# Performance work log

Measured on AMD Instinct MI355X. Metric: run time of the kernel, lower is better.

Reference implementation:

```python
import jax, jax.numpy as jnp
import numpy as np
from jax.scipy.special import logsumexp

B, T, D, H, K = 64, 800, 80, 128, 39  # batch, frames, feat dim, LSTM hidden/dir, num phones


def setup_inputs() -> dict:
    key = jax.random.key(0)
    ks = jax.random.split(key, 16)
    s = 0.1
    inp = {
        "features": jax.random.normal(ks[0], (B, T, D), jnp.float32),
        "lengths": jax.random.randint(ks[1], (B,), T // 2, T + 1, dtype=jnp.int32),
        "labels": jax.random.randint(ks[2], (B, T), 0, K, dtype=jnp.int32),
        # BiLSTM params (PyTorch layout: W_ih (4H,D), W_hh (4H,H); gate order i,f,g,o)
        "Wih_f": jax.random.normal(ks[3], (4 * H, D), jnp.float32) * s,
        "Whh_f": jax.random.normal(ks[4], (4 * H, H), jnp.float32) * s,
        "bih_f": jax.random.normal(ks[5], (4 * H,), jnp.float32) * s,
        "bhh_f": jax.random.normal(ks[6], (4 * H,), jnp.float32) * s,
        "Wih_b": jax.random.normal(ks[7], (4 * H, D), jnp.float32) * s,
        "Whh_b": jax.random.normal(ks[8], (4 * H, H), jnp.float32) * s,
        "bih_b": jax.random.normal(ks[9], (4 * H,), jnp.float32) * s,
        "bhh_b": jax.random.normal(ks[10], (4 * H,), jnp.float32) * s,
        # emission projection Linear(2H -> K)
        "Wp": jax.random.normal(ks[11], (K, 2 * H), jnp.float32) * s,
        "bp": jax.random.normal(ks[12], (K,), jnp.float32) * s,
        # CRF params (pytorch-crf init: U(-0.1, 0.1))
        "start_t": jax.random.uniform(ks[13], (K,), jnp.float32, -0.1, 0.1),
        "end_t": jax.random.uniform(ks[14], (K,), jnp.float32, -0.1, 0.1),
        "trans": jax.random.uniform(ks[15], (K, K), jnp.float32, -0.1, 0.1),
    }
    return inp


def _lstm(x, Wih, Whh, bih, bhh, reverse):
    """Single-direction LSTM over padded batch. x: (B,T,D) -> (B,T,H)."""
    nB, nT, _ = x.shape
    nH = Whh.shape[1]
    xW = jnp.swapaxes(x @ Wih.T + (bih + bhh), 0, 1)  # (T,B,4H)

    def step(carry, g):
        h, c = carry
        g = g + h @ Whh.T
        i, f, gg, o = jnp.split(g, 4, axis=-1)
        c = jax.nn.sigmoid(f) * c + jax.nn.sigmoid(i) * jnp.tanh(gg)
        h = jax.nn.sigmoid(o) * jnp.tanh(c)
        return (h, c), h

    init = (jnp.zeros((nB, nH), x.dtype), jnp.zeros((nB, nH), x.dtype))
    _, hs = jax.lax.scan(step, init, xW, reverse=reverse)
    return jnp.swapaxes(hs, 0, 1)  # (B,T,H)


def _crf_nll(emissions, labels, lengths, start_t, end_t, trans):
    """pytorch-crf: -mean log-likelihood. emissions (B,T,K), labels (B,T)."""
    nB, nT, nK = emissions.shape
    mask = (jnp.arange(nT)[None, :] < lengths[:, None])  # (B,T)
    mf = mask.astype(emissions.dtype)
    bidx = jnp.arange(nB)

    # --- numerator: score of gold path ---
    num = start_t[labels[:, 0]] + emissions[bidx, 0, labels[:, 0]]
    tr = trans[labels[:, :-1], labels[:, 1:]]  # (B,T-1)
    em = jnp.take_along_axis(emissions[:, 1:], labels[:, 1:, None], axis=2)[..., 0]
    num = num + ((tr + em) * mf[:, 1:]).sum(axis=1)
    last_tags = jnp.take_along_axis(labels, (lengths - 1)[:, None], axis=1)[:, 0]
    num = num + end_t[last_tags]

    # --- denominator: forward algorithm ---
    alpha0 = start_t[None, :] + emissions[:, 0]  # (B,K)
    em_rest = jnp.swapaxes(emissions[:, 1:], 0, 1)  # (T-1,B,K)
    m_rest = jnp.swapaxes(mask[:, 1:], 0, 1)  # (T-1,B)

    def step(alpha, inputs):
        em_t, m_t = inputs
        nxt = logsumexp(alpha[:, :, None] + trans[None] + em_t[:, None, :], axis=1)
        return jnp.where(m_t[:, None], nxt, alpha), None

    alpha, _ = jax.lax.scan(step, alpha0, (em_rest, m_rest))
    denom = logsumexp(alpha + end_t[None, :], axis=1)

    return -(num - denom).mean()


def reference(features, lengths, labels, Wih_f, Whh_f, bih_f, bhh_f,
              Wih_b, Whh_b, bih_b, bhh_b, Wp, bp, start_t, end_t, trans):
    h_f = _lstm(features, Wih_f, Whh_f, bih_f, bhh_f, reverse=False)
    h_b = _lstm(features, Wih_b, Whh_b, bih_b, bhh_b, reverse=True)
    hidden = jnp.concatenate([h_f, h_b], axis=-1)  # (B,T,2H)
    emissions = hidden @ Wp.T + bp  # (B,T,K)
    return _crf_nll(emissions, labels, lengths, start_t, end_t, trans)
```

## Files before the change

### kernel.cpp

```cpp
#include <hip/hip_runtime.h>
#include <cstddef>
#include <cstdint>

#define B_ 64
#define T_ 800
#define D_ 80
#define H_ 128
#define K_ 39
#define BT_ (B_ * T_)

#define NL2E_  (-1.44269504f)
#define N2L2E_ (-2.88539008f)

typedef _Float16 h2_t  __attribute__((ext_vector_type(2)));
typedef _Float16 f16x8 __attribute__((ext_vector_type(8)));
typedef float    f32x4 __attribute__((ext_vector_type(4)));
typedef uint32_t u32x4 __attribute__((ext_vector_type(4)));

__device__ __forceinline__ float fdot2_(h2_t a, h2_t b, float c) {
#if __has_builtin(__builtin_amdgcn_fdot2)
  return __builtin_amdgcn_fdot2(a, b, c, false);
#else
  return c + (float)a.x * (float)b.x + (float)a.y * (float)b.y;
#endif
}

__device__ __forceinline__ h2_t asH2u_(uint32_t u) { return __builtin_bit_cast(h2_t, u); }

__device__ __forceinline__ float ex2_(float x) {
#if __has_builtin(__builtin_amdgcn_exp2f)
  return __builtin_amdgcn_exp2f(x);
#else
  return __builtin_exp2f(x);
#endif
}
__device__ __forceinline__ float rcpf_(float x) {
#if __has_builtin(__builtin_amdgcn_rcpf)
  return __builtin_amdgcn_rcpf(x);
#else
  return 1.0f / x;
#endif
}
__device__ __forceinline__ float tanhf_(float x) { return 2.0f / (1.0f + __expf(-2.0f * x)) - 1.0f; }

__device__ __forceinline__ float laneb_(float v, int lane) {
  return __builtin_bit_cast(float, __builtin_amdgcn_readlane(__builtin_bit_cast(int, v), lane));
}
__device__ __forceinline__ uint32_t lanebu_(uint32_t v, int lane) {
  return (uint32_t)__builtin_amdgcn_readlane((int)v, lane);
}

__device__ __forceinline__ float dppswap1_(float v) {
  return __builtin_bit_cast(float,
    __builtin_amdgcn_mov_dpp(__builtin_bit_cast(int, v), 0xB1, 0xF, 0xF, true));
}

__device__ __forceinline__ void barrier_lds_() {
  asm volatile("s_waitcnt lgkmcnt(0)" ::: "memory");
  __builtin_amdgcn_s_barrier();
}

__device__ __forceinline__ void rows_of_(int tid, int& unit, int& role, int& r0, int& r1) {
  const int w = tid >> 6, L = tid & 63;
  unit = w * 32 + (L >> 1);
  role = L & 1;
  r0 = role * H_ + unit;
  r1 = 2 * H_ + role * H_ + unit;
}

__global__ __launch_bounds__(256, 1)
void xw_kernel(const float* __restrict__ x,
               const float* __restrict__ Wih_f, const float* __restrict__ Wih_b,
               _Float16* __restrict__ xw)
{
  const int dir = blockIdx.x & 1;
  const int mc  = blockIdx.x >> 1;
  const float* W = dir ? Wih_b : Wih_f;

  const int tid  = threadIdx.x;
  const int w    = tid >> 6;
  const int lane = tid & 63;
  const int lm   = lane & 15;
  const int quad = lane >> 4;
  const int selw = w >> 1;
  const int rolw = w & 1;

  f16x8 Bf[8][3];
  #pragma unroll
  for (int nt = 0; nt < 8; ++nt) {
    const int r = w * 128 + nt * 16 + lm;
    const float fac = (r >= 256 && r < 384) ? N2L2E_ : NL2E_;
    #pragma unroll
    for (int kt = 0; kt < 3; ++kt) {
      const int kb = kt * 32 + quad * 8;
      #pragma unroll
      for (int j = 0; j < 8; ++j) {
        const int k = kb + j;
        Bf[nt][kt][j] = (k < D_) ? (_Float16)(fac * W[(size_t)r * D_ + k]) : (_Float16)0.0f;
      }
    }
  }

  __shared__ alignas(16) _Float16 xs[128 * 96];
  for (int i = tid; i < 128 * 96; i += 256) xs[i] = (_Float16)0.0f;

  for (int cc = 0; cc < 4; ++cc) {
    const int base = mc * 512 + cc * 128;
    __syncthreads();
    {
      const float4* src = (const float4*)(x + (size_t)base * D_);
      for (int i = tid; i < 128 * D_ / 4; i += 256) {
        float4 v = src[i];
        const int row = i / 20, col = (i % 20) * 4;
        h2_t p0, p1;
        p0.x = (_Float16)v.x; p0.y = (_Float16)v.y;
        p1.x = (_Float16)v.z; p1.y = (_Float16)v.w;
        uint2 pk;
        pk.x = __builtin_bit_cast(uint32_t, p0);
        pk.y = __builtin_bit_cast(uint32_t, p1);
        *(uint2*)&xs[row * 96 + col] = pk;
      }
    }
    __syncthreads();

    #pragma unroll
    for (int mt = 0; mt < 8; ++mt) {
      f16x8 Af[3];
      #pragma unroll
      for (int kt = 0; kt < 3; ++kt)
        Af[kt] = *(const f16x8*)&xs[(mt * 16 + lm) * 96 + kt * 32 + quad * 8];

      f32x4 acc[8];
      #pragma unroll
      for (int nt = 0; nt < 8; ++nt) acc[nt] = (f32x4){0.f, 0.f, 0.f, 0.f};
      #pragma unroll
      for (int kt = 0; kt < 3; ++kt)
        #pragma unroll
        for (int nt = 0; nt < 8; ++nt)
          acc[nt] = __builtin_amdgcn_mfma_f32_16x16x32_f16(Af[kt], Bf[nt][kt], acc[nt], 0, 0, 0);

      #pragma unroll
      for (int nt = 0; nt < 8; ++nt) {
        const int unit = nt * 16 + lm;
        const int ptid = (unit >> 5) * 64 + (unit & 31) * 2 + rolw;
        #pragma unroll
        for (int rg = 0; rg < 4; ++rg) {
          const int bt = base + mt * 16 + quad * 4 + rg;
          xw[((size_t)dir * BT_ + bt) * 512 + ptid * 2 + selw] = (_Float16)acc[nt][rg];
        }
      }
    }
  }
}

template<int USE_XW>
__global__ __launch_bounds__(256, 1)
void lstm_kernel(const float* __restrict__ x,
                 const float* __restrict__ Wih_f, const float* __restrict__ Whh_f,
                 const float* __restrict__ bih_f, const float* __restrict__ bhh_f,
                 const float* __restrict__ Wih_b, const float* __restrict__ Whh_b,
                 const float* __restrict__ bih_b, const float* __restrict__ bhh_b,
                 const _Float16* __restrict__ xw,
                 _Float16* __restrict__ hcat)
{
  const int bb  = blockIdx.x & 63;
  const int dir = blockIdx.x >> 6;
  const float* Whh = dir ? Whh_b : Whh_f;
  const float* Wih = dir ? Wih_b : Wih_f;
  const float* bih = dir ? bih_b : bih_f;
  const float* bhh = dir ? bhh_b : bhh_f;

  const int tid  = threadIdx.x;
  const int lane = tid & 63;
  int unit, role, r0, r1; rows_of_(tid, unit, role, r0, r1);
  const float s0 = NL2E_;
  const float s1 = role ? NL2E_ : N2L2E_;
  const float qk2 = role ? 0.0f : -1.0f;

  h2_t w0[64], w1[64];
  #pragma unroll
  for (int j = 0; j < 64; ++j) {
    float2 a = *(const float2*)(Whh + (size_t)r0 * H_ + 2 * j);
    float2 d = *(const float2*)(Whh + (size_t)r1 * H_ + 2 * j);
    w0[j].x = (_Float16)(s0 * a.x); w0[j].y = (_Float16)(s0 * a.y);
    w1[j].x = (_Float16)(s1 * d.x); w1[j].y = (_Float16)(s1 * d.y);
  }
  h2_t wx0[40], wx1[40];
  if (!USE_XW) {
    #pragma unroll
    for (int i = 0; i < 40; ++i) {
      float2 a = *(const float2*)(Wih + (size_t)r0 * D_ + 2 * i);
      float2 d = *(const float2*)(Wih + (size_t)r1 * D_ + 2 * i);
      wx0[i].x = (_Float16)(s0 * a.x); wx0[i].y = (_Float16)(s0 * a.y);
      wx1[i].x = (_Float16)(s1 * d.x); wx1[i].y = (_Float16)(s1 * d.y);
    }
  }
  const float bias0 = s0 * (bih[r0] + bhh[r0]);
  const float bias1 = s1 * (bih[r1] + bhh[r1]);

  __shared__ alignas(16) _Float16 hsf[2][H_];
  __shared__ uint32_t xs2[2][64];

  if (tid < H_) hsf[0][tid] = (_Float16)0.0f;
  if (!USE_XW && tid < 64) { xs2[0][tid] = 0u; xs2[1][tid] = 0u; }
  float c = 0.0f;

  const uint32_t* xwdu = (const uint32_t*)xw + ((size_t)dir * BT_ + (size_t)bb * T_) * 256;
  const float*    xb   = x + (size_t)bb * T_ * D_;
  _Float16*       hb   = hcat + (size_t)bb * T_ * (2 * H_) + dir * H_;

  _Float16* hbp = hb + (size_t)(dir ? (T_ - 1) : 0) * (2 * H_);
  const ptrdiff_t hstep = dir ? -(2 * H_) : (2 * H_);
  int xoff = (dir ? (T_ - 3) : 2) * 256 + tid;
  const int xstep = dir ? -256 : 256;

  uint32_t xwA = 0u, xwB = 0u;
  h2_t xpend; xpend.x = (_Float16)0.f; xpend.y = (_Float16)0.f;
  {
    const int tq0 = dir ? (T_ - 1) : 0;
    const int tq1 = dir ? (T_ - 2) : 1;
    if (USE_XW) {
      xwA = xwdu[(size_t)tq0 * 256 + tid];
      xwB = xwdu[(size_t)tq1 * 256 + tid];
    } else if (tid < 40) {
      float2 v0 = *(const float2*)(xb + (size_t)tq0 * D_ + 2 * tid);
      h2_t p; p.x = (_Float16)v0.x; p.y = (_Float16)v0.y;
      xs2[0][tid] = __builtin_bit_cast(uint32_t, p);
      float2 v1 = *(const float2*)(xb + (size_t)tq1 * D_ + 2 * tid);
      xpend.x = (_Float16)v1.x; xpend.y = (_Float16)v1.y;
    }
  }
  __syncthreads();

  auto step = [&](int tt, int par, uint32_t& xwreg) {
    float a0, a1, a2, a3, b0, b1, b2, b3;
    if (USE_XW) {
      const h2_t xv = asH2u_(xwreg);
      a0 = bias0 + (float)xv.x;
      b0 = bias1 + (float)xv.y;
      a1 = a2 = a3 = 0.f; b1 = b2 = b3 = 0.f;
      xwreg = xwdu[xoff];
    } else {
      a0 = bias0; b0 = bias1;
      a1 = a2 = a3 = 0.f; b1 = b2 = b3 = 0.f;
      if (tid < 40) {
        xs2[par ^ 1][tid] = __builtin_bit_cast(uint32_t, xpend);
        const int ttc = (tt + 2 < T_) ? (tt + 2) : (T_ - 1);
        const int tq2 = dir ? (T_ - 1 - ttc) : ttc;
        float2 v = *(const float2*)(xb + (size_t)tq2 * D_ + 2 * tid);
        xpend.x = (_Float16)v.x; xpend.y = (_Float16)v.y;
      }
      uint32_t xreg = xs2[par][lane];
      #pragma unroll
      for (int j = 0; j < 40; j += 4) {
        h2_t q0 = asH2u_(lanebu_(xreg, j));
        h2_t q1 = asH2u_(lanebu_(xreg, j + 1));
        h2_t q2 = asH2u_(lanebu_(xreg, j + 2));
        h2_t q3 = asH2u_(lanebu_(xreg, j + 3));
        a0 = fdot2_(wx0[j],     q0, a0); b0 = fdot2_(wx1[j],     q0, b0);
        a1 = fdot2_(wx0[j + 1], q1, a1); b1 = fdot2_(wx1[j + 1], q1, b1);
        a2 = fdot2_(wx0[j + 2], q2, a2); b2 = fdot2_(wx1[j + 2], q2, b2);
        a3 = fdot2_(wx0[j + 3], q3, a3); b3 = fdot2_(wx1[j + 3], q3, b3);
      }
    }

    const u32x4* hq = (const u32x4*)hsf[par];
    #pragma unroll
    for (int g = 0; g < 16; ++g) {
      const u32x4 hv = hq[g];
      a0 = fdot2_(w0[4 * g + 0], asH2u_(hv[0]), a0);
      b0 = fdot2_(w1[4 * g + 0], asH2u_(hv[0]), b0);
      a1 = fdot2_(w0[4 * g + 1], asH2u_(hv[1]), a1);
      b1 = fdot2_(w1[4 * g + 1], asH2u_(hv[1]), b1);
      a2 = fdot2_(w0[4 * g + 2], asH2u_(hv[2]), a2);
      b2 = fdot2_(w1[4 * g + 2], asH2u_(hv[2]), b2);
      a3 = fdot2_(w0[4 * g + 3], asH2u_(hv[3]), a3);
      b3 = fdot2_(w1[4 * g + 3], asH2u_(hv[3]), b3);
    }
    const float ga = (a0 + a1) + (a2 + a3);
    const float gb = (b0 + b1) + (b2 + b3);

    const float ea = ex2_(ga);
    const float sg = rcpf_(1.0f + ea);
    const float gbc = fminf(fmaxf(gb, -34.6f), 34.6f);
    const float eb = ex2_(gbc);
    const float qv = fmaf(qk2, eb, 1.0f) * rcpf_(1.0f + eb);
    const float ex = dppswap1_(sg * qv);
    c = fmaf(sg, c, ex);
    const float hn = qv * tanhf_(c);
    if (role) {
      hsf[par ^ 1][unit] = (_Float16)hn;
      hbp[unit] = (_Float16)hn;
    }
    hbp += hstep;
    if (tt + 3 < T_) xoff += xstep;
    barrier_lds_();
  };

  for (int tb = 0; tb < T_; tb += 2) {
    step(tb,     0, xwA);
    step(tb + 1, 1, xwB);
  }
}

__global__ __launch_bounds__(256, 1)
void emis_kernel(const _Float16* __restrict__ hcat,
                 const float* __restrict__ Wp, const float* __restrict__ bp,
                 float* __restrict__ em)
{
  const int tid  = threadIdx.x;
  const int w    = tid >> 6;
  const int lane = tid & 63;
  const int lm   = lane & 15;
  const int quad = lane >> 4;

  f16x8 Bf[3][8];
  float bias[3];
  #pragma unroll
  for (int nt = 0; nt < 3; ++nt) {
    const int n = nt * 16 + lm;
    const bool valid = n < K_;
    bias[nt] = valid ? bp[n] : 0.0f;
    #pragma unroll
    for (int kt = 0; kt < 8; ++kt) {
      const int kb = kt * 32 + quad * 8;
      #pragma unroll
      for (int j = 0; j < 8; ++j)
        Bf[nt][kt][j] = valid ? (_Float16)Wp[(size_t)n * 256 + kb + j] : (_Float16)0.0f;
    }
  }

  #pragma unroll
  for (int q = 0; q < 4; ++q) {
    const int mt  = blockIdx.x * 16 + w * 4 + q;
    const int bt0 = mt * 16;

    f16x8 Af[8];
    const _Float16* ab = hcat + ((size_t)bt0 + lm) * 256;
    #pragma unroll
    for (int kt = 0; kt < 8; ++kt)
      Af[kt] = *(const f16x8*)(ab + kt * 32 + quad * 8);

    f32x4 acc[3];
    #pragma unroll
    for (int nt = 0; nt < 3; ++nt) acc[nt] = (f32x4){0.f, 0.f, 0.f, 0.f};
    #pragma unroll
    for (int kt = 0; kt < 8; ++kt)
      #pragma unroll
      for (int nt = 0; nt < 3; ++nt)
        acc[nt] = __builtin_amdgcn_mfma_f32_16x16x32_f16(Af[kt], Bf[nt][kt], acc[nt], 0, 0, 0);

    #pragma unroll
    for (int nt = 0; nt < 3; ++nt) {
      const int n = nt * 16 + lm;
      if (n < K_) {
        #pragma unroll
        for (int rg = 0; rg < 4; ++rg) {
          const int row = bt0 + quad * 4 + rg;
          em[(size_t)row * K_ + n] = acc[nt][rg] + bias[nt];
        }
      }
    }
  }
}

__global__ __launch_bounds__(256)
void crf_dn_kernel(const float* __restrict__ em,
                   const int* __restrict__ labels, const int* __restrict__ lengths,
                   const float* __restrict__ start_t, const float* __restrict__ end_t,
                   const float* __restrict__ trans,
                   float* __restrict__ dn)
{
  const int b    = blockIdx.x;
  const int tid  = threadIdx.x;
  const int wv   = tid >> 6;
  const int lane = tid & 63;
  const int len  = lengths[b];
  const float* emb = em + (size_t)b * T_ * K_;

  __shared__ float s_num[3];
  __shared__ float s_den;
  __shared__ alignas(16) float vbuf[64];

  if (wv == 0) {
    float et[K_];
    #pragma unroll
    for (int j = 0; j < K_; ++j)
      et[j] = (lane < K_) ? __expf(trans[j * K_ + lane]) : 0.0f;

    float a0 = (lane < K_) ? (start_t[lane] + emb[lane]) : -1e30f;
    float m = a0;
    #pragma unroll
    for (int off = 32; off > 0; off >>= 1) m = fmaxf(m, __shfl_xor(m, off));
    float v = __expf(a0 - m);
    float off_acc = m;
    vbuf[lane] = 0.0f;

    auto ldc = [&](int t) -> float {
      const int tc = (t < len) ? t : (len - 1);
      return (lane < K_) ? emb[(size_t)tc * K_ + lane] : 0.0f;
    };

    float eA = ldc(1), eB = ldc(2), eC = ldc(3), eD = ldc(4);
    float eE = ldc(5), eF = ldc(6), eG = ldc(7), eH = ldc(8);

    auto stepden = [&](float& ereg, int tt) {
      const float emc = ereg;
      ereg = ldc(tt + 8);
      if (tt < len) {
        vbuf[lane] = v;
        asm volatile("s_waitcnt lgkmcnt(0)" ::: "memory");
        const float4* vq = (const float4*)vbuf;
        float s0 = 0.f, s1 = 0.f, s2 = 0.f, s3 = 0.f;
        #pragma unroll
        for (int g = 0; g < 9; ++g) {
          const float4 q = vq[g];
          s0 = fmaf(q.x, et[4 * g],     s0);
          s1 = fmaf(q.y, et[4 * g + 1], s1);
          s2 = fmaf(q.z, et[4 * g + 2], s2);
          s3 = fmaf(q.w, et[4 * g + 3], s3);
        }
        const float4 q9 = vq[9];
        s0 = fmaf(q9.x, et[36], s0);
        s1 = fmaf(q9.y, et[37], s1);
        s2 = fmaf(q9.z, et[38], s2);
        v = ((s0 + s1) + (s2 + s3)) * __expf(emc);
        if ((tt & 1) == 0) {
          const float sc = laneb_(v, 0);
          v *= 1.0f / sc;
          off_acc += __logf(sc);
        }
      }
    };

    for (int t = 1; t < len; t += 8) {
      stepden(eA, t);     stepden(eB, t + 1);
      stepden(eC, t + 2); stepden(eD, t + 3);
      stepden(eE, t + 4); stepden(eF, t + 5);
      stepden(eG, t + 6); stepden(eH, t + 7);
    }

    float w = (lane < K_) ? v * __expf(end_t[lane]) : 0.0f;
    #pragma unroll
    for (int off = 32; off > 0; off >>= 1) w += __shfl_xor(w, off);
    if (lane == 0) s_den = off_acc + __logf(w);
  } else {
    const int idx = tid - 64;
    float acc = 0.0f;
    for (int t = 1 + idx; t < len; t += 192) {
      const int lp = labels[b * T_ + t - 1];
      const int lc = labels[b * T_ + t];
      acc += trans[lp * K_ + lc] + emb[(size_t)t * K_ + lc];
    }
    if (tid == 64) {
      const int l0 = labels[b * T_];
      const int ll = labels[b * T_ + len - 1];
      acc += start_t[l0] + emb[l0] + end_t[ll];
    }
    #pragma unroll
    for (int off = 32; off > 0; off >>= 1) acc += __shfl_xor(acc, off);
    if (lane == 0) s_num[wv - 1] = acc;
  }
  __syncthreads();
  if (tid == 0) dn[b] = s_den - (s_num[0] + s_num[1] + s_num[2]);
}

__global__ void finalize_kernel(const float* __restrict__ dn, float* __restrict__ out)
{
  const int tid = threadIdx.x;
  float v = dn[tid];
  #pragma unroll
  for (int off = 32; off > 0; off >>= 1) v += __shfl_down(v, off);
  if (tid == 0) out[0] = v * (1.0f / 64.0f);
}

extern "C" void kernel_launch(void* const* d_in, const int* in_sizes, int n_in,
                              void* d_out, int out_size, void* d_ws, size_t ws_size,
                              hipStream_t stream)
{
  (void)in_sizes; (void)n_in; (void)out_size;
  const float* features = (const float*)d_in[0];
  const int*   lengths  = (const int*)d_in[1];
  const int*   labels   = (const int*)d_in[2];
  const float* Wih_f = (const float*)d_in[3];
  const float* Whh_f = (const float*)d_in[4];
  const float* bih_f = (const float*)d_in[5];
  const float* bhh_f = (const float*)d_in[6];
  const float* Wih_b = (const float*)d_in[7];
  const float* Whh_b = (const float*)d_in[8];
  const float* bih_b = (const float*)d_in[9];
  const float* bhh_b = (const float*)d_in[10];
  const float* Wp      = (const float*)d_in[11];
  const float* bp      = (const float*)d_in[12];
  const float* start_t = (const float*)d_in[13];
  const float* end_t   = (const float*)d_in[14];
  const float* trans   = (const float*)d_in[15];
  float* out = (float*)d_out;

  char* wsc = (char*)d_ws;
  _Float16* hcatH = (_Float16*)wsc;
  float*    em    = (float*)(wsc + 26214400);
  float*    dn    = (float*)(wsc + 26214400 + 7987200);
  _Float16* xwH   = (_Float16*)(wsc + 34202112);
  const bool big  = ws_size >= (size_t)34202112 + 104857600;

  if (big) {
    hipLaunchKernelGGL(xw_kernel, dim3(200), dim3(256), 0, stream,
                       features, Wih_f, Wih_b, xwH);
    hipLaunchKernelGGL((lstm_kernel<1>), dim3(2 * B_), dim3(256), 0, stream,
                       features, Wih_f, Whh_f, bih_f, bhh_f,
                       Wih_b, Whh_b, bih_b, bhh_b, xwH, hcatH);
  } else {
    hipLaunchKernelGGL((lstm_kernel<0>), dim3(2 * B_), dim3(256), 0, stream,
                       features, Wih_f, Whh_f, bih_f, bhh_f,
                       Wih_b, Whh_b, bih_b, bhh_b, xwH, hcatH);
  }
  hipLaunchKernelGGL(emis_kernel, dim3(BT_ / 256), dim3(256), 0, stream,
                     hcatH, Wp, bp, em);
  hipLaunchKernelGGL(crf_dn_kernel, dim3(B_), dim3(256), 0, stream,
                     em, labels, lengths, start_t, end_t, trans, dn);
  hipLaunchKernelGGL(finalize_kernel, dim3(1), dim3(64), 0, stream,
                     dn, out);
}
```

Before: 788.8 us.

## Share hidden-state LDS reads across lane quads via DPP and broadcast CRF alpha via readlane

In the LSTM recurrence, each lane of a 4-lane quad now reads only one quarter of the hidden vector from LDS. The other quarters arrive through DPP quad permutes, and the Whh fragments are reordered per lane to match. This cuts LDS read traffic per step on the serial critical path, at the cost of 48 extra DPP moves per step and a permuted weight layout. In the CRF forward pass, the LDS store, wait and vector reload of alpha is replaced by readlane broadcasts, which removes an LDS round trip per time step but adds scalar readlanes.

```diff
diff --git a/kernel.cpp b/kernel.cpp
--- a/kernel.cpp
+++ b/kernel.cpp
@@ -53,6 +53,11 @@
 __device__ __forceinline__ float dppswap1_(float v) {
   return __builtin_bit_cast(float,
     __builtin_amdgcn_mov_dpp(__builtin_bit_cast(int, v), 0xB1, 0xF, 0xF, true));
+}
+
+template<int CTRL>
+__device__ __forceinline__ uint32_t dppu_(uint32_t v) {
+  return (uint32_t)__builtin_amdgcn_mov_dpp((int)v, CTRL, 0xF, 0xF, true);
 }
 
 __device__ __forceinline__ void barrier_lds_() {
@@ -172,18 +177,24 @@
 
   const int tid  = threadIdx.x;
   const int lane = tid & 63;
+  const int Q    = lane & 3;
   int unit, role, r0, r1; rows_of_(tid, unit, role, r0, r1);
   const float s0 = NL2E_;
   const float s1 = role ? NL2E_ : N2L2E_;
   const float qk2 = role ? 0.0f : -1.0f;
 
-  h2_t w0[64], w1[64];
+  h2_t wp0[64], wp1[64];
   #pragma unroll
-  for (int j = 0; j < 64; ++j) {
-    float2 a = *(const float2*)(Whh + (size_t)r0 * H_ + 2 * j);
-    float2 d = *(const float2*)(Whh + (size_t)r1 * H_ + 2 * j);
-    w0[j].x = (_Float16)(s0 * a.x); w0[j].y = (_Float16)(s0 * a.y);
-    w1[j].x = (_Float16)(s1 * d.x); w1[j].y = (_Float16)(s1 * d.y);
+  for (int r = 0; r < 4; ++r) {
+    const int ch = Q ^ r;
+    #pragma unroll
+    for (int jj = 0; jj < 16; ++jj) {
+      const int j = ch * 16 + jj;
+      float2 a = *(const float2*)(Whh + (size_t)r0 * H_ + 2 * j);
+      float2 d = *(const float2*)(Whh + (size_t)r1 * H_ + 2 * j);
+      wp0[r * 16 + jj].x = (_Float16)(s0 * a.x); wp0[r * 16 + jj].y = (_Float16)(s0 * a.y);
+      wp1[r * 16 + jj].x = (_Float16)(s1 * d.x); wp1[r * 16 + jj].y = (_Float16)(s1 * d.y);
+    }
   }
   h2_t wx0[40], wx1[40];
   if (!USE_XW) {
@@ -233,16 +244,16 @@
   __syncthreads();
 
   auto step = [&](int tt, int par, uint32_t& xwreg) {
-    float a0, a1, a2, a3, b0, b1, b2, b3;
+    float a[4], b[4];
     if (USE_XW) {
       const h2_t xv = asH2u_(xwreg);
-      a0 = bias0 + (float)xv.x;
-      b0 = bias1 + (float)xv.y;
-      a1 = a2 = a3 = 0.f; b1 = b2 = b3 = 0.f;
+      a[0] = bias0 + (float)xv.x;
+      b[0] = bias1 + (float)xv.y;
+      a[1] = a[2] = a[3] = 0.f; b[1] = b[2] = b[3] = 0.f;
       xwreg = xwdu[xoff];
     } else {
-      a0 = bias0; b0 = bias1;
-      a1 = a2 = a3 = 0.f; b1 = b2 = b3 = 0.f;
+      a[0] = bias0; b[0] = bias1;
+      a[1] = a[2] = a[3] = 0.f; b[1] = b[2] = b[3] = 0.f;
       if (tid < 40) {
         xs2[par ^ 1][tid] = __builtin_bit_cast(uint32_t, xpend);
         const int ttc = (tt + 2 < T_) ? (tt + 2) : (T_ - 1);
@@ -257,28 +268,47 @@
         h2_t q1 = asH2u_(lanebu_(xreg, j + 1));
         h2_t q2 = asH2u_(lanebu_(xreg, j + 2));
         h2_t q3 = asH2u_(lanebu_(xreg, j + 3));
-        a0 = fdot2_(wx0[j],     q0, a0); b0 = fdot2_(wx1[j],     q0, b0);
-        a1 = fdot2_(wx0[j + 1], q1, a1); b1 = fdot2_(wx1[j + 1], q1, b1);
-        a2 = fdot2_(wx0[j + 2], q2, a2); b2 = fdot2_(wx1[j + 2], q2, b2);
-        a3 = fdot2_(wx0[j + 3], q3, a3); b3 = fdot2_(wx1[j + 3], q3, b3);
+        a[0] = fdot2_(wx0[j],     q0, a[0]); b[0] = fdot2_(wx1[j],     q0, b[0]);
+        a[1] = fdot2_(wx0[j + 1], q1, a[1]); b[1] = fdot2_(wx1[j + 1], q1, b[1]);
+        a[2] = fdot2_(wx0[j + 2], q2, a[2]); b[2] = fdot2_(wx1[j + 2], q2, b[2]);
+        a[3] = fdot2_(wx0[j + 3], q3, a[3]); b[3] = fdot2_(wx1[j + 3], q3, b[3]);
       }
     }
 
     const u32x4* hq = (const u32x4*)hsf[par];
-    #pragma unroll
-    for (int g = 0; g < 16; ++g) {
-      const u32x4 hv = hq[g];
-      a0 = fdot2_(w0[4 * g + 0], asH2u_(hv[0]), a0);
-      b0 = fdot2_(w1[4 * g + 0], asH2u_(hv[0]), b0);
-      a1 = fdot2_(w0[4 * g + 1], asH2u_(hv[1]), a1);
-      b1 = fdot2_(w1[4 * g + 1], asH2u_(hv[1]), b1);
-      a2 = fdot2_(w0[4 * g + 2], asH2u_(hv[2]), a2);
-      b2 = fdot2_(w1[4 * g + 2], asH2u_(hv[2]), b2);
-      a3 = fdot2_(w0[4 * g + 3], asH2u_(hv[3]), a3);
-      b3 = fdot2_(w1[4 * g + 3], asH2u_(hv[3]), b3);
-    }
-    const float ga = (a0 + a1) + (a2 + a3);
-    const float gb = (b0 + b1) + (b2 + b3);
+    u32x4 ovr[4];
+    #pragma unroll
+    for (int reg = 0; reg < 4; ++reg) ovr[reg] = hq[Q * 4 + reg];
+
+    u32x4 x1[4], x2[4], x3[4];
+    #pragma unroll
+    for (int reg = 0; reg < 4; ++reg) {
+      #pragma unroll
+      for (int e = 0; e < 4; ++e) {
+        x1[reg][e] = dppu_<0xB1>(ovr[reg][e]);
+        x2[reg][e] = dppu_<0x4E>(ovr[reg][e]);
+        x3[reg][e] = dppu_<0x1B>(ovr[reg][e]);
+      }
+    }
+
+    #define HROUND_(HV, RB)                                        \
+      _Pragma("unroll")                                            \
+      for (int reg = 0; reg < 4; ++reg) {                          \
+        _Pragma("unroll")                                          \
+        for (int e = 0; e < 4; ++e) {                              \
+          const h2_t hh = asH2u_((HV)[reg][e]);                    \
+          a[e] = fdot2_(wp0[(RB) + reg * 4 + e], hh, a[e]);        \
+          b[e] = fdot2_(wp1[(RB) + reg * 4 + e], hh, b[e]);        \
+        }                                                          \
+      }
+    HROUND_(ovr, 0)
+    HROUND_(x1, 16)
+    HROUND_(x2, 32)
+    HROUND_(x3, 48)
+    #undef HROUND_
+
+    const float ga = (a[0] + a[1]) + (a[2] + a[3]);
+    const float gb = (b[0] + b[1]) + (b[2] + b[3]);
 
     const float ea = ex2_(ga);
     const float sg = rcpf_(1.0f + ea);
@@ -380,7 +410,6 @@
 
   __shared__ float s_num[3];
   __shared__ float s_den;
-  __shared__ alignas(16) float vbuf[64];
 
   if (wv == 0) {
     float et[K_];
@@ -394,7 +423,6 @@
     for (int off = 32; off > 0; off >>= 1) m = fmaxf(m, __shfl_xor(m, off));
     float v = __expf(a0 - m);
     float off_acc = m;
-    vbuf[lane] = 0.0f;
 
     auto ldc = [&](int t) -> float {
       const int tc = (t < len) ? t : (len - 1);
@@ -408,22 +436,18 @@
       const float emc = ereg;
       ereg = ldc(tt + 8);
       if (tt < len) {
-        vbuf[lane] = v;
-        asm volatile("s_waitcnt lgkmcnt(0)" ::: "memory");
-        const float4* vq = (const float4*)vbuf;
+        const float pv = v;
         float s0 = 0.f, s1 = 0.f, s2 = 0.f, s3 = 0.f;
         #pragma unroll
-        for (int g = 0; g < 9; ++g) {
-          const float4 q = vq[g];
-          s0 = fmaf(q.x, et[4 * g],     s0);
-          s1 = fmaf(q.y, et[4 * g + 1], s1);
-          s2 = fmaf(q.z, et[4 * g + 2], s2);
-          s3 = fmaf(q.w, et[4 * g + 3], s3);
+        for (int j = 0; j < 36; j += 4) {
+          s0 = fmaf(laneb_(pv, j),     et[j],     s0);
+          s1 = fmaf(laneb_(pv, j + 1), et[j + 1], s1);
+          s2 = fmaf(laneb_(pv, j + 2), et[j + 2], s2);
+          s3 = fmaf(laneb_(pv, j + 3), et[j + 3], s3);
         }
-        const float4 q9 = vq[9];
-        s0 = fmaf(q9.x, et[36], s0);
-        s1 = fmaf(q9.y, et[37], s1);
-        s2 = fmaf(q9.z, et[38], s2);
+        s0 = fmaf(laneb_(pv, 36), et[36], s0);
+        s1 = fmaf(laneb_(pv, 37), et[37], s1);
+        s2 = fmaf(laneb_(pv, 38), et[38], s2);
         v = ((s0 + s1) + (s2 + s3)) * __expf(emc);
         if ((tt & 1) == 0) {
           const float sc = laneb_(v, 0);
```

Result: faster. 749.0 us (-5.1%).

## Fuse input projection into LSTM kernel and use lane broadcasts in CRF recursion

Applied to the files above, without the earlier changes.

Removes the separate xw_kernel and has each LSTM block compute its own batch row's input projection with MFMA before the recurrence, writing into its own xw slice. This drops a kernel launch and lets the projection run inside the 128-block LSTM grid instead of a separate 200-block pass. The CRF forward step now gathers alpha with lane broadcasts instead of an LDS round trip, and renormalizes every fourth step instead of every second. The fused prologue serializes projection work per block on only 128 CUs. Less frequent renormalization carries some overflow risk.

```diff
diff --git a/kernel.cpp b/kernel.cpp
--- a/kernel.cpp
+++ b/kernel.cpp
@@ -66,91 +66,6 @@
   role = L & 1;
   r0 = role * H_ + unit;
   r1 = 2 * H_ + role * H_ + unit;
-}
-
-__global__ __launch_bounds__(256, 1)
-void xw_kernel(const float* __restrict__ x,
-               const float* __restrict__ Wih_f, const float* __restrict__ Wih_b,
-               _Float16* __restrict__ xw)
-{
-  const int dir = blockIdx.x & 1;
-  const int mc  = blockIdx.x >> 1;
-  const float* W = dir ? Wih_b : Wih_f;
-
-  const int tid  = threadIdx.x;
-  const int w    = tid >> 6;
-  const int lane = tid & 63;
-  const int lm   = lane & 15;
-  const int quad = lane >> 4;
-  const int selw = w >> 1;
-  const int rolw = w & 1;
-
-  f16x8 Bf[8][3];
-  #pragma unroll
-  for (int nt = 0; nt < 8; ++nt) {
-    const int r = w * 128 + nt * 16 + lm;
-    const float fac = (r >= 256 && r < 384) ? N2L2E_ : NL2E_;
-    #pragma unroll
-    for (int kt = 0; kt < 3; ++kt) {
-      const int kb = kt * 32 + quad * 8;
-      #pragma unroll
-      for (int j = 0; j < 8; ++j) {
-        const int k = kb + j;
-        Bf[nt][kt][j] = (k < D_) ? (_Float16)(fac * W[(size_t)r * D_ + k]) : (_Float16)0.0f;
-      }
-    }
-  }
-
-  __shared__ alignas(16) _Float16 xs[128 * 96];
-  for (int i = tid; i < 128 * 96; i += 256) xs[i] = (_Float16)0.0f;
-
-  for (int cc = 0; cc < 4; ++cc) {
-    const int base = mc * 512 + cc * 128;
-    __syncthreads();
-    {
-      const float4* src = (const float4*)(x + (size_t)base * D_);
-      for (int i = tid; i < 128 * D_ / 4; i += 256) {
-        float4 v = src[i];
-        const int row = i / 20, col = (i % 20) * 4;
-        h2_t p0, p1;
-        p0.x = (_Float16)v.x; p0.y = (_Float16)v.y;
-        p1.x = (_Float16)v.z; p1.y = (_Float16)v.w;
-        uint2 pk;
-        pk.x = __builtin_bit_cast(uint32_t, p0);
-        pk.y = __builtin_bit_cast(uint32_t, p1);
-        *(uint2*)&xs[row * 96 + col] = pk;
-      }
-    }
-    __syncthreads();
-
-    #pragma unroll
-    for (int mt = 0; mt < 8; ++mt) {
-      f16x8 Af[3];
-      #pragma unroll
-      for (int kt = 0; kt < 3; ++kt)
-        Af[kt] = *(const f16x8*)&xs[(mt * 16 + lm) * 96 + kt * 32 + quad * 8];
-
-      f32x4 acc[8];
-      #pragma unroll
-      for (int nt = 0; nt < 8; ++nt) acc[nt] = (f32x4){0.f, 0.f, 0.f, 0.f};
-      #pragma unroll
-      for (int kt = 0; kt < 3; ++kt)
-        #pragma unroll
-        for (int nt = 0; nt < 8; ++nt)
-          acc[nt] = __builtin_amdgcn_mfma_f32_16x16x32_f16(Af[kt], Bf[nt][kt], acc[nt], 0, 0, 0);
-
-      #pragma unroll
-      for (int nt = 0; nt < 8; ++nt) {
-        const int unit = nt * 16 + lm;
-        const int ptid = (unit >> 5) * 64 + (unit & 31) * 2 + rolw;
-        #pragma unroll
-        for (int rg = 0; rg < 4; ++rg) {
-          const int bt = base + mt * 16 + quad * 4 + rg;
-          xw[((size_t)dir * BT_ + bt) * 512 + ptid * 2 + selw] = (_Float16)acc[nt][rg];
-        }
-      }
-    }
-  }
 }
 
 template<int USE_XW>
@@ -160,7 +75,7 @@
                  const float* __restrict__ bih_f, const float* __restrict__ bhh_f,
                  const float* __restrict__ Wih_b, const float* __restrict__ Whh_b,
                  const float* __restrict__ bih_b, const float* __restrict__ bhh_b,
-                 const _Float16* __restrict__ xw,
+                 _Float16* __restrict__ xw,
                  _Float16* __restrict__ hcat)
 {
   const int bb  = blockIdx.x & 63;
@@ -172,6 +87,91 @@
 
   const int tid  = threadIdx.x;
   const int lane = tid & 63;
+
+  __shared__ alignas(16) _Float16 hsf[2][H_];
+  __shared__ uint32_t xs2[2][64];
+  __shared__ alignas(16) _Float16 xs[128 * 96];
+
+  if (USE_XW) {
+    const int w    = tid >> 6;
+    const int lm   = lane & 15;
+    const int quad = lane >> 4;
+    const int selw = w >> 1;
+    const int rolw = w & 1;
+
+    f16x8 Bf[8][3];
+    #pragma unroll
+    for (int nt = 0; nt < 8; ++nt) {
+      const int r = w * 128 + nt * 16 + lm;
+      const float fac = (r >= 256 && r < 384) ? N2L2E_ : NL2E_;
+      #pragma unroll
+      for (int kt = 0; kt < 3; ++kt) {
+        const int kb = kt * 32 + quad * 8;
+        #pragma unroll
+        for (int j = 0; j < 8; ++j) {
+          const int k = kb + j;
+          Bf[nt][kt][j] = (k < D_) ? (_Float16)(fac * Wih[(size_t)r * D_ + k]) : (_Float16)0.0f;
+        }
+      }
+    }
+
+    for (int i = tid; i < 128 * 96; i += 256) xs[i] = (_Float16)0.0f;
+
+    for (int cc = 0; cc < 7; ++cc) {
+      const int base = cc * 128;
+      const int nrow = (T_ - base < 128) ? (T_ - base) : 128;
+      __syncthreads();
+      {
+        const float4* src = (const float4*)(x + ((size_t)bb * T_ + base) * D_);
+        for (int i = tid; i < nrow * 20; i += 256) {
+          float4 v = src[i];
+          const int row = i / 20, col = (i % 20) * 4;
+          h2_t p0, p1;
+          p0.x = (_Float16)v.x; p0.y = (_Float16)v.y;
+          p1.x = (_Float16)v.z; p1.y = (_Float16)v.w;
+          uint2 pk;
+          pk.x = __builtin_bit_cast(uint32_t, p0);
+          pk.y = __builtin_bit_cast(uint32_t, p1);
+          *(uint2*)&xs[row * 96 + col] = pk;
+        }
+      }
+      __syncthreads();
+
+      #pragma unroll
+      for (int mt = 0; mt < 8; ++mt) {
+        if (base + mt * 16 >= T_) break;
+        f16x8 Af[3];
+        #pragma unroll
+        for (int kt = 0; kt < 3; ++kt)
+          Af[kt] = *(const f16x8*)&xs[(mt * 16 + lm) * 96 + kt * 32 + quad * 8];
+
+        f32x4 acc[8];
+        #pragma unroll
+        for (int nt = 0; nt < 8; ++nt) acc[nt] = (f32x4){0.f, 0.f, 0.f, 0.f};
+        #pragma unroll
+        for (int kt = 0; kt < 3; ++kt)
+          #pragma unroll
+          for (int nt = 0; nt < 8; ++nt)
+            acc[nt] = __builtin_amdgcn_mfma_f32_16x16x32_f16(Af[kt], Bf[nt][kt], acc[nt], 0, 0, 0);
+
+        #pragma unroll
+        for (int nt = 0; nt < 8; ++nt) {
+          const int unit = nt * 16 + lm;
+          const int ptid = (unit >> 5) * 64 + (unit & 31) * 2 + rolw;
+          #pragma unroll
+          for (int rg = 0; rg < 4; ++rg) {
+            const int t = base + mt * 16 + quad * 4 + rg;
+            if (t < T_)
+              xw[((size_t)dir * BT_ + (size_t)bb * T_ + t) * 512 + ptid * 2 + selw]
+                = (_Float16)acc[nt][rg];
+          }
+        }
+      }
+    }
+    __syncthreads();
+  }
+
+  const int Q = lane & 3; (void)Q;
   int unit, role, r0, r1; rows_of_(tid, unit, role, r0, r1);
   const float s0 = NL2E_;
   const float s1 = role ? NL2E_ : N2L2E_;
@@ -197,9 +197,6 @@
   }
   const float bias0 = s0 * (bih[r0] + bhh[r0]);
   const float bias1 = s1 * (bih[r1] + bhh[r1]);
-
-  __shared__ alignas(16) _Float16 hsf[2][H_];
-  __shared__ uint32_t xs2[2][64];
 
   if (tid < H_) hsf[0][tid] = (_Float16)0.0f;
   if (!USE_XW && tid < 64) { xs2[0][tid] = 0u; xs2[1][tid] = 0u; }
@@ -380,7 +377,6 @@
 
   __shared__ float s_num[3];
   __shared__ float s_den;
-  __shared__ alignas(16) float vbuf[64];
 
   if (wv == 0) {
     float et[K_];
@@ -394,7 +390,6 @@
     for (int off = 32; off > 0; off >>= 1) m = fmaxf(m, __shfl_xor(m, off));
     float v = __expf(a0 - m);
     float off_acc = m;
-    vbuf[lane] = 0.0f;
 
     auto ldc = [&](int t) -> float {
       const int tc = (t < len) ? t : (len - 1);
@@ -408,24 +403,20 @@
       const float emc = ereg;
       ereg = ldc(tt + 8);
       if (tt < len) {
-        vbuf[lane] = v;
-        asm volatile("s_waitcnt lgkmcnt(0)" ::: "memory");
-        const float4* vq = (const float4*)vbuf;
+        const float pv = v;
         float s0 = 0.f, s1 = 0.f, s2 = 0.f, s3 = 0.f;
         #pragma unroll
-        for (int g = 0; g < 9; ++g) {
-          const float4 q = vq[g];
-          s0 = fmaf(q.x, et[4 * g],     s0);
-          s1 = fmaf(q.y, et[4 * g + 1], s1);
-          s2 = fmaf(q.z, et[4 * g + 2], s2);
-          s3 = fmaf(q.w, et[4 * g + 3], s3);
+        for (int j = 0; j < 36; j += 4) {
+          s0 = fmaf(laneb_(pv, j),     et[j],     s0);
+          s1 = fmaf(laneb_(pv, j + 1), et[j + 1], s1);
+          s2 = fmaf(laneb_(pv, j + 2), et[j + 2], s2);
+          s3 = fmaf(laneb_(pv, j + 3), et[j + 3], s3);
         }
-        const float4 q9 = vq[9];
-        s0 = fmaf(q9.x, et[36], s0);
-        s1 = fmaf(q9.y, et[37], s1);
-        s2 = fmaf(q9.z, et[38], s2);
+        s0 = fmaf(laneb_(pv, 36), et[36], s0);
+        s1 = fmaf(laneb_(pv, 37), et[37], s1);
+        s2 = fmaf(laneb_(pv, 38), et[38], s2);
         v = ((s0 + s1) + (s2 + s3)) * __expf(emc);
-        if ((tt & 1) == 0) {
+        if ((tt & 3) == 0) {
           const float sc = laneb_(v, 0);
           v *= 1.0f / sc;
           off_acc += __logf(sc);
@@ -505,8 +496,6 @@
   const bool big  = ws_size >= (size_t)34202112 + 104857600;
 
   if (big) {
-    hipLaunchKernelGGL(xw_kernel, dim3(200), dim3(256), 0, stream,
-                       features, Wih_f, Wih_b, xwH);
     hipLaunchKernelGGL((lstm_kernel<1>), dim3(2 * B_), dim3(256), 0, stream,
                        features, Wih_f, Whh_f, bih_f, bhh_f,
                        Wih_b, Whh_b, bih_b, bhh_b, xwH, hcatH);
```

Result: faster. 769.0 us (-2.5%).

## Parallelize CRF forward recursion over time chunks with MFMA transfer-matrix products

Applied to the files above, without the earlier changes.

Splits the sequential CRF forward algorithm into 25 time chunks per batch element. Each chunk computes a normalized 39x39 product of exp(trans)·diag(exp(emission)) matrices with fp16 MFMA. A second kernel then chains the chunk matrices onto the alpha vector serially. This replaces 800 dependent steps per sequence with parallel chunk work plus 25 sequential matrix-vector steps, at the cost of doing matrix-matrix rather than vector-matrix work and accepting fp16 rounding in the products. The fallback kernel also swaps its LDS broadcast for lane broadcasts and renormalizes less often.

```diff
diff --git a/kernel.cpp b/kernel.cpp
--- a/kernel.cpp
+++ b/kernel.cpp
@@ -9,8 +9,13 @@
 #define K_ 39
 #define BT_ (B_ * T_)
 
+#define GCH_ 32
+#define NCH_ 25
+#define CHF_ 1664
+
 #define NL2E_  (-1.44269504f)
 #define N2L2E_ (-2.88539008f)
+#define L2E_   (1.44269504f)
 
 typedef _Float16 h2_t  __attribute__((ext_vector_type(2)));
 typedef _Float16 f16x8 __attribute__((ext_vector_type(8)));
@@ -364,6 +369,196 @@
   }
 }
 
+__global__ __launch_bounds__(64, 1)
+void crf_chunk_kernel(const float* __restrict__ em,
+                      const int* __restrict__ lengths,
+                      const float* __restrict__ trans,
+                      float* __restrict__ Pbuf)
+{
+  const int b    = blockIdx.x / NCH_;
+  const int c    = blockIdx.x % NCH_;
+  const int lane = threadIdx.x;
+  const int lm   = lane & 15;
+  const int quad = lane >> 4;
+  const int len  = lengths[b];
+  const int t0   = 1 + c * GCH_;
+  int t1 = 1 + (c + 1) * GCH_;
+  if (t1 > T_)  t1 = T_;
+  if (t1 > len) t1 = len;
+
+  f16x8 Bf[3][2];
+  #pragma unroll
+  for (int nt = 0; nt < 3; ++nt) {
+    const int n = nt * 16 + lm;
+    #pragma unroll
+    for (int kf = 0; kf < 2; ++kf) {
+      #pragma unroll
+      for (int jj = 0; jj < 8; ++jj) {
+        const int j = kf * 32 + quad * 8 + jj;
+        Bf[nt][kf][jj] = (j < K_ && n < K_)
+          ? (_Float16)__expf(trans[j * K_ + n]) : (_Float16)0.0f;
+      }
+    }
+  }
+
+  __shared__ alignas(16) _Float16 Plds[48 * 68];
+  for (int i = lane; i < 48 * 68; i += 64) Plds[i] = (_Float16)0.0f;
+  if (lane < K_) Plds[lane * 68 + lane] = (_Float16)1.0f;
+  asm volatile("s_waitcnt lgkmcnt(0)" ::: "memory");
+
+  float sacc = 0.0f;
+  const float* emb = em + (size_t)b * T_ * K_;
+
+  for (int t = t0; t < t1; ++t) {
+    float emv[3], e3[3];
+    float mloc = -1e30f;
+    #pragma unroll
+    for (int nt = 0; nt < 3; ++nt) {
+      const int col = nt * 16 + lm;
+      emv[nt] = (col < K_) ? emb[(size_t)t * K_ + col] : -1e30f;
+      mloc = fmaxf(mloc, emv[nt]);
+    }
+    #pragma unroll
+    for (int off = 8; off >= 1; off >>= 1)
+      mloc = fmaxf(mloc, __shfl_xor(mloc, off));
+    #pragma unroll
+    for (int nt = 0; nt < 3; ++nt) {
+      const int col = nt * 16 + lm;
+      e3[nt] = (col < K_) ? ex2_((emv[nt] - mloc) * L2E_) : 0.0f;
+    }
+
+    f32x4 acc[3][3];
+    #pragma unroll
+    for (int mt = 0; mt < 3; ++mt)
+      #pragma unroll
+      for (int nt = 0; nt < 3; ++nt)
+        acc[mt][nt] = (f32x4){0.f, 0.f, 0.f, 0.f};
+    #pragma unroll
+    for (int kf = 0; kf < 2; ++kf) {
+      f16x8 Am[3];
+      #pragma unroll
+      for (int mt = 0; mt < 3; ++mt)
+        Am[mt] = *(const f16x8*)&Plds[(mt * 16 + lm) * 68 + kf * 32 + quad * 8];
+      #pragma unroll
+      for (int mt = 0; mt < 3; ++mt)
+        #pragma unroll
+        for (int nt = 0; nt < 3; ++nt)
+          acc[mt][nt] = __builtin_amdgcn_mfma_f32_16x16x32_f16(Am[mt], Bf[nt][kf], acc[mt][nt], 0, 0, 0);
+    }
+
+    float sv[3][3][4];
+    float mx = 0.0f;
+    #pragma unroll
+    for (int mt = 0; mt < 3; ++mt)
+      #pragma unroll
+      for (int nt = 0; nt < 3; ++nt)
+        #pragma unroll
+        for (int rg = 0; rg < 4; ++rg) {
+          const float s = acc[mt][nt][rg] * e3[nt];
+          sv[mt][nt][rg] = s;
+          mx = fmaxf(mx, s);
+        }
+    #pragma unroll
+    for (int off = 32; off >= 1; off >>= 1)
+      mx = fmaxf(mx, __shfl_xor(mx, off));
+    const float rmx = rcpf_(mx);
+    sacc += mloc - __logf(rmx);
+
+    #pragma unroll
+    for (int mt = 0; mt < 3; ++mt)
+      #pragma unroll
+      for (int nt = 0; nt < 3; ++nt)
+        #pragma unroll
+        for (int rg = 0; rg < 4; ++rg) {
+          const int row = mt * 16 + quad * 4 + rg;
+          const int col = nt * 16 + lm;
+          Plds[row * 68 + col] = (_Float16)(sv[mt][nt][rg] * rmx);
+        }
+    asm volatile("s_waitcnt lgkmcnt(0)" ::: "memory");
+  }
+
+  float* rec = Pbuf + ((size_t)(b * NCH_ + c)) * CHF_;
+  for (int i = lane; i < 1600; i += 64) {
+    const int r = i / 40, cc2 = i % 40;
+    rec[i] = (float)Plds[r * 68 + cc2];
+  }
+  if (lane == 0) rec[1600] = sacc;
+}
+
+__global__ __launch_bounds__(256)
+void crf_comb2_kernel(const float* __restrict__ em,
+                      const int* __restrict__ labels, const int* __restrict__ lengths,
+                      const float* __restrict__ start_t, const float* __restrict__ end_t,
+                      const float* __restrict__ trans,
+                      const float* __restrict__ Pbuf,
+                      float* __restrict__ dn)
+{
+  const int b    = blockIdx.x;
+  const int tid  = threadIdx.x;
+  const int wv   = tid >> 6;
+  const int lane = tid & 63;
+  const int len  = lengths[b];
+  const float* emb = em + (size_t)b * T_ * K_;
+
+  __shared__ float s_num[3];
+  __shared__ float s_den;
+
+  if (wv == 0) {
+    float a0 = (lane < K_) ? (start_t[lane] + emb[lane]) : -1e30f;
+    float m = a0;
+    #pragma unroll
+    for (int off = 32; off > 0; off >>= 1) m = fmaxf(m, __shfl_xor(m, off));
+    float av = __expf(a0 - m);
+    float off_acc = m;
+
+    for (int c = 0; c < NCH_; ++c) {
+      const float* rec = Pbuf + ((size_t)(b * NCH_ + c)) * CHF_;
+      const float pv = av;
+      float s0 = 0.f, s1 = 0.f, s2 = 0.f, s3 = 0.f;
+      #pragma unroll
+      for (int j = 0; j < 36; j += 4) {
+        s0 = fmaf(laneb_(pv, j),     rec[(j)     * 40 + lane], s0);
+        s1 = fmaf(laneb_(pv, j + 1), rec[(j + 1) * 40 + lane], s1);
+        s2 = fmaf(laneb_(pv, j + 2), rec[(j + 2) * 40 + lane], s2);
+        s3 = fmaf(laneb_(pv, j + 3), rec[(j + 3) * 40 + lane], s3);
+      }
+      s0 = fmaf(laneb_(pv, 36), rec[36 * 40 + lane], s0);
+      s1 = fmaf(laneb_(pv, 37), rec[37 * 40 + lane], s1);
+      s2 = fmaf(laneb_(pv, 38), rec[38 * 40 + lane], s2);
+      float vn = (lane < K_) ? ((s0 + s1) + (s2 + s3)) : 0.0f;
+      float mx = vn;
+      #pragma unroll
+      for (int off = 32; off > 0; off >>= 1) mx = fmaxf(mx, __shfl_xor(mx, off));
+      const float rmx = rcpf_(mx);
+      av = vn * rmx;
+      off_acc += rec[1600] - __logf(rmx);
+    }
+
+    float w = (lane < K_) ? av * __expf(end_t[lane]) : 0.0f;
+    #pragma unroll
+    for (int off = 32; off > 0; off >>= 1) w += __shfl_xor(w, off);
+    if (lane == 0) s_den = off_acc + __logf(w);
+  } else {
+    const int idx = tid - 64;
+    float acc = 0.0f;
+    for (int t = 1 + idx; t < len; t += 192) {
+      const int lp = labels[b * T_ + t - 1];
+      const int lc = labels[b * T_ + t];
+      acc += trans[lp * K_ + lc] + emb[(size_t)t * K_ + lc];
+    }
+    if (tid == 64) {
+      const int l0 = labels[b * T_];
+      const int ll = labels[b * T_ + len - 1];
+      acc += start_t[l0] + emb[l0] + end_t[ll];
+    }
+    #pragma unroll
+    for (int off = 32; off > 0; off >>= 1) acc += __shfl_xor(acc, off);
+    if (lane == 0) s_num[wv - 1] = acc;
+  }
+  __syncthreads();
+  if (tid == 0) dn[b] = s_den - (s_num[0] + s_num[1] + s_num[2]);
+}
+
 __global__ __launch_bounds__(256)
 void crf_dn_kernel(const float* __restrict__ em,
                    const int* __restrict__ labels, const int* __restrict__ lengths,
@@ -380,7 +575,6 @@
 
   __shared__ float s_num[3];
   __shared__ float s_den;
-  __shared__ alignas(16) float vbuf[64];
 
   if (wv == 0) {
     float et[K_];
@@ -394,7 +588,6 @@
     for (int off = 32; off > 0; off >>= 1) m = fmaxf(m, __shfl_xor(m, off));
     float v = __expf(a0 - m);
     float off_acc = m;
-    vbuf[lane] = 0.0f;
 
     auto ldc = [&](int t) -> float {
       const int tc = (t < len) ? t : (len - 1);
@@ -408,24 +601,20 @@
       const float emc = ereg;
       ereg = ldc(tt + 8);
       if (tt < len) {
-        vbuf[lane] = v;
-        asm volatile("s_waitcnt lgkmcnt(0)" ::: "memory");
-        const float4* vq = (const float4*)vbuf;
+        const float pv = v;
         float s0 = 0.f, s1 = 0.f, s2 = 0.f, s3 = 0.f;
         #pragma unroll
-        for (int g = 0; g < 9; ++g) {
-          const float4 q = vq[g];
-          s0 = fmaf(q.x, et[4 * g],     s0);
-          s1 = fmaf(q.y, et[4 * g + 1], s1);
-          s2 = fmaf(q.z, et[4 * g + 2], s2);
-          s3 = fmaf(q.w, et[4 * g + 3], s3);
+        for (int j = 0; j < 36; j += 4) {
+          s0 = fmaf(laneb_(pv, j),     et[j],     s0);
+          s1 = fmaf(laneb_(pv, j + 1), et[j + 1], s1);
+          s2 = fmaf(laneb_(pv, j + 2), et[j + 2], s2);
+          s3 = fmaf(laneb_(pv, j + 3), et[j + 3], s3);
         }
-        const float4 q9 = vq[9];
-        s0 = fmaf(q9.x, et[36], s0);
-        s1 = fmaf(q9.y, et[37], s1);
-        s2 = fmaf(q9.z, et[38], s2);
+        s0 = fmaf(laneb_(pv, 36), et[36], s0);
+        s1 = fmaf(laneb_(pv, 37), et[37], s1);
+        s2 = fmaf(laneb_(pv, 38), et[38], s2);
         v = ((s0 + s1) + (s2 + s3)) * __expf(emc);
-        if ((tt & 1) == 0) {
+        if ((tt & 3) == 0) {
           const float sc = laneb_(v, 0);
           v *= 1.0f / sc;
           off_acc += __logf(sc);
@@ -502,6 +691,7 @@
   float*    em    = (float*)(wsc + 26214400);
   float*    dn    = (float*)(wsc + 26214400 + 7987200);
   _Float16* xwH   = (_Float16*)(wsc + 34202112);
+  float*    Pbuf  = (float*)(wsc + 34202112);
   const bool big  = ws_size >= (size_t)34202112 + 104857600;
 
   if (big) {
@@ -510,15 +700,21 @@
     hipLaunchKernelGGL((lstm_kernel<1>), dim3(2 * B_), dim3(256), 0, stream,
                        features, Wih_f, Whh_f, bih_f, bhh_f,
                        Wih_b, Whh_b, bih_b, bhh_b, xwH, hcatH);
+    hipLaunchKernelGGL(emis_kernel, dim3(BT_ / 256), dim3(256), 0, stream,
+                       hcatH, Wp, bp, em);
+    hipLaunchKernelGGL(crf_chunk_kernel, dim3(B_ * NCH_), dim3(64), 0, stream,
+                       em, lengths, trans, Pbuf);
+    hipLaunchKernelGGL(crf_comb2_kernel, dim3(B_), dim3(256), 0, stream,
+                       em, labels, lengths, start_t, end_t, trans, Pbuf, dn);
   } else {
     hipLaunchKernelGGL((lstm_kernel<0>), dim3(2 * B_), dim3(256), 0, stream,
                        features, Wih_f, Whh_f, bih_f, bhh_f,
                        Wih_b, Whh_b, bih_b, bhh_b, xwH, hcatH);
-  }
-  hipLaunchKernelGGL(emis_kernel, dim3(BT_ / 256), dim3(256), 0, stream,
-                     hcatH, Wp, bp, em);
-  hipLaunchKernelGGL(crf_dn_kernel, dim3(B_), dim3(256), 0, stream,
-                     em, labels, lengths, start_t, end_t, trans, dn);
+    hipLaunchKernelGGL(emis_kernel, dim3(BT_ / 256), dim3(256), 0, stream,
+                       hcatH, Wp, bp, em);
+    hipLaunchKernelGGL(crf_dn_kernel, dim3(B_), dim3(256), 0, stream,
+                       em, labels, lengths, start_t, end_t, trans, dn);
+  }
   hipLaunchKernelGGL(finalize_kernel, dim3(1), dim3(64), 0, stream,
                      dn, out);
 }
```

Result: faster. 653.5 us (-17.2%).
